# Kernel tuning notes

Measured on AMD Instinct MI355X. Metric: run time of the kernel, lower is better.

Reference implementation:

```python
import jax, jax.numpy as jnp
import numpy as np

N, C, T, V, S = 64, 64, 300, 25, 3
INTER = C // 4  # coff_embedding = 4
KER_T = 9      # temporal attention kernel
KER_V = V      # V=25 is odd -> spatial attention kernel = V, pad = (V-1)//2


def setup_inputs() -> dict:
    key = jax.random.key(0)
    ks = jax.random.split(key, 20)
    f = lambda k, s, scale=0.05: jax.random.normal(k, s, jnp.float32) * scale
    return {
        "x": jax.random.normal(ks[0], (N, C, T, V), jnp.float32),
        "A": f(ks[1], (S, V, V), 0.2),
        "alpha": jnp.array(0.1, jnp.float32),
        "Wa": f(ks[2], (S, INTER, C)), "ba": f(ks[3], (S, INTER)),
        "Wb": f(ks[4], (S, INTER, C)), "bb": f(ks[5], (S, INTER)),
        "Wd": f(ks[6], (S, C, C)),     "bd": f(ks[7], (S, C)),
        "bn_gamma": jnp.ones((C,), jnp.float32),
        "bn_beta": jnp.zeros((C,), jnp.float32),
        "bn_mean": f(ks[8], (C,)),
        "bn_var": jax.random.uniform(ks[9], (C,), jnp.float32) + 0.5,
        "Wsa": f(ks[10], (1, C, KER_V)), "bsa": f(ks[11], (1,)),
        "Wta": f(ks[12], (1, C, KER_T)), "bta": f(ks[13], (1,)),
        "Wfc1": f(ks[14], (C // 2, C)),  "bfc1": f(ks[15], (C // 2,)),
        "Wfc2": f(ks[16], (C, C // 2)),  "bfc2": f(ks[17], (C,)),
    }


def _conv1d(z, w, bias, pad):
    # z: [N, Cin, L], w: [Cout, Cin, K] -> [N, Cout, L]
    o = jax.lax.conv_general_dilated(z, w, (1,), [(pad, pad)],
                                     dimension_numbers=('NCH', 'OIH', 'NCH'))
    return o + bias[None, :, None]


def reference(x, A, alpha, Wa, ba, Wb, bb, Wd, bd,
              bn_gamma, bn_beta, bn_mean, bn_var,
              Wsa, bsa, Wta, bta, Wfc1, bfc1, Wfc2, bfc2):
    n, c, t, v = x.shape
    inter = Wa.shape[1]
    # adaptive adjacency per subset (1x1 convs = channel einsums)
    a = jnp.einsum('nctv,sic->nsitv', x, Wa) + ba[None, :, :, None, None]   # [N,S,inter,T,V]
    b = jnp.einsum('nctv,sic->nsitv', x, Wb) + bb[None, :, :, None, None]
    M = jnp.tanh(jnp.einsum('nsitv,nsitw->nsvw', a, b) / (inter * t))       # [N,S,V,V]
    G = A[None] + alpha * M
    # graph conv: x @ G per subset, then 1x1 conv_d, summed over subsets
    zp = jnp.einsum('nctv,nsvw->nsctw', x, G)                                # [N,S,C,T,V]
    y = jnp.einsum('nsctv,soc->notv', zp, Wd) + bd.sum(0)[None, :, None, None]
    # BN (eval) + residual (down = identity since in_c == out_c) + ReLU
    inv = bn_gamma / jnp.sqrt(bn_var + 1e-5)
    y = (y - bn_mean[None, :, None, None]) * inv[None, :, None, None] + bn_beta[None, :, None, None]
    y = jax.nn.relu(y + x)
    # spatial attention over joints
    se1 = jax.nn.sigmoid(_conv1d(y.mean(2), Wsa, bsa, (KER_V - 1) // 2))    # [N,1,V]
    y = y * se1[:, :, None, :] + y
    # temporal attention over frames
    se1 = jax.nn.sigmoid(_conv1d(y.mean(3), Wta, bta, (KER_T - 1) // 2))    # [N,1,T]
    y = y * se1[:, :, :, None] + y
    # channel attention (squeeze-excite)
    se = y.mean((2, 3))                                                      # [N,C]
    se2 = jax.nn.sigmoid(jax.nn.relu(se @ Wfc1.T + bfc1) @ Wfc2.T + bfc2)
    y = y * se2[:, :, None, None] + y
    return y
```

## Files before the change

### kernel.cpp

```cpp
#include <hip/hip_runtime.h>

typedef __bf16 bf16;
typedef bf16 bf16x8 __attribute__((ext_vector_type(8)));
typedef bf16 bf16x4 __attribute__((ext_vector_type(4)));
typedef float f32x4 __attribute__((ext_vector_type(4)));
typedef short s16x4 __attribute__((ext_vector_type(4)));

#define WS_XG    0u
#define WS_WAB   61505536u
#define WS_WD    61517824u
#define WS_COEFA 61542400u
#define WS_COEFB 61542656u
#define WS_GT    61542912u
#define WS_MPART 61936128u
#define WS_STP   61936128u
#define WS_SVP   68489728u
#define WS_SE1   74519040u
#define WS_SE2   74527232u
#define WS_SE3   74605056u

__device__ __forceinline__ f32x4 mfma16(bf16x8 a, bf16x8 b, f32x4 c) {
  return __builtin_amdgcn_mfma_f32_16x16x32_bf16(a, b, c, 0, 0, 0);
}

#if __has_builtin(__builtin_amdgcn_mfma_f32_16x16x16_bf16)
__device__ __forceinline__ f32x4 mfma16k(bf16x4 a, bf16x4 b, f32x4 c) {
  return __builtin_amdgcn_mfma_f32_16x16x16_bf16(a, b, c, 0, 0, 0);
}
#elif __has_builtin(__builtin_amdgcn_mfma_f32_16x16x16bf16_1k)
__device__ __forceinline__ f32x4 mfma16k(bf16x4 a, bf16x4 b, f32x4 c) {
  s16x4 ai = __builtin_bit_cast(s16x4, a);
  s16x4 bi = __builtin_bit_cast(s16x4, b);
  return __builtin_amdgcn_mfma_f32_16x16x16bf16_1k(ai, bi, c, 0, 0, 0);
}
#else
__device__ __forceinline__ f32x4 mfma16k(bf16x4 a, bf16x4 b, f32x4 c) {
  asm volatile("v_mfma_f32_16x16x16_bf16 %0, %1, %2, %0" : "+v"(c) : "v"(a), "v"(b));
  return c;
}
#endif

__global__ __launch_bounds__(256) void k_prep(
    const float* __restrict__ Wa, const float* __restrict__ Wb,
    const float* __restrict__ Wd, const float* __restrict__ bd,
    const float* __restrict__ gam, const float* __restrict__ bet,
    const float* __restrict__ mean, const float* __restrict__ var,
    char* __restrict__ ws) {
  bf16* wab = (bf16*)(ws + WS_WAB);
  bf16* wd  = (bf16*)(ws + WS_WD);
  float* cA = (float*)(ws + WS_COEFA);
  float* cB = (float*)(ws + WS_COEFB);
  int tid = threadIdx.x;
  for (int f = tid; f < 3*32*64; f += 256) {
    int s = f >> 11, r = (f >> 6) & 31, c = f & 63;
    float v = (r < 16) ? Wa[(s*16 + r)*64 + c] : Wb[(s*16 + (r-16))*64 + c];
    wab[f] = (bf16)v;
  }
  for (int f = tid; f < 3*64*64; f += 256) wd[f] = (bf16)Wd[f];
  if (tid < 64) {
    float bds = bd[tid] + bd[64+tid] + bd[128+tid];
    float iv = gam[tid] / sqrtf(var[tid] + 1e-5f);
    cA[tid] = iv;
    cB[tid] = (bds - mean[tid]) * iv + bet[tid];
  }
}

__global__ __launch_bounds__(256) void k_tr(
    const float* __restrict__ x, char* __restrict__ ws) {
  __shared__ __attribute__((aligned(16))) bf16 tile[64*204];
  const int tc = blockIdx.x, n = blockIdx.y, tid = threadIdx.x;
  const int t0 = tc*8;
  const int vmax = min(200, 7500 - t0*25);
  bf16* XG = (bf16*)(ws + WS_XG);
  #pragma unroll
  for (int it = 0; it < 13; ++it) {
    int u = it*256 + tid;
    if (u < 3200) {
      int c = u / 50, q = u % 50;
      int idx = 4*q;
      if (idx < vmax) {
        float4 val = *(const float4*)(x + (size_t)(n*64 + c)*7500 + t0*25 + idx);
        bf16x4 pk = {(bf16)val.x, (bf16)val.y, (bf16)val.z, (bf16)val.w};
        *(bf16x4*)&tile[c*204 + idx] = pk;
      }
    }
  }
  __syncthreads();
  #pragma unroll
  for (int it = 0; it < 7; ++it) {
    int u = it*256 + tid;
    if (u < 1600) {
      int c8 = u & 7, tv = u >> 3;
      int t = t0 + tv/25, v = tv % 25;
      if (t < 300) {
        bf16x8 pk;
        #pragma unroll
        for (int j = 0; j < 8; ++j) pk[j] = tile[(c8*8 + j)*204 + tv];
        *(bf16x8*)&XG[((size_t)(n*300 + t)*25 + v)*64 + c8*8] = pk;
      }
    }
  }
}

__global__ __launch_bounds__(256, 3) void k1_m(
    const float* __restrict__ ba_g, const float* __restrict__ bb_g,
    char* __restrict__ ws) {
  __shared__ float red[4][32][33];
  const int seg = blockIdx.x, n = blockIdx.y;
  const int tid = threadIdx.x;
  const int lane = tid & 63, wv = tid >> 6;
  const int l15 = lane & 15, l4 = lane >> 4;
  const int t0 = seg*19, tlen = min(19, 300 - t0);
  const bf16* XG  = (const bf16*)(ws + WS_XG);
  const bf16* wab = (const bf16*)(ws + WS_WAB);
  const f32x4 z4 = {0.f,0.f,0.f,0.f};

  bf16x8 Afr[6][2];
  float bias[6][4];
  #pragma unroll
  for (int rt = 0; rt < 6; ++rt) {
    const int s = rt >> 1, abk = rt & 1;
    #pragma unroll
    for (int kk = 0; kk < 2; ++kk)
      Afr[rt][kk] = *(const bf16x8*)&wab[(s*32 + abk*16 + l15)*64 + kk*32 + 8*l4];
    const float* bp = abk ? bb_g : ba_g;
    #pragma unroll
    for (int r = 0; r < 4; ++r) bias[rt][r] = bp[s*16 + 4*l4 + r];
  }
  f32x4 macc[3][2][2] = {};
  const int tb = (tlen*wv) >> 2, te = (tlen*(wv+1)) >> 2;

  for (int tl = tb; tl < te; ++tl) {
    const size_t rowb = (size_t)(n*300 + t0 + tl)*25;
    bf16x8 Bv[2][2];
    #pragma unroll
    for (int vt = 0; vt < 2; ++vt)
      #pragma unroll
      for (int kk = 0; kk < 2; ++kk)
        Bv[vt][kk] = *(const bf16x8*)&XG[(rowb + vt*16 + l15)*64 + kk*32 + 8*l4];
    #pragma unroll
    for (int s = 0; s < 3; ++s) {
      f32x4 acc[2][2];
      #pragma unroll
      for (int ab = 0; ab < 2; ++ab)
        #pragma unroll
        for (int vt = 0; vt < 2; ++vt) {
          f32x4 a = mfma16(Afr[2*s + ab][0], Bv[vt][0], z4);
          acc[ab][vt] = mfma16(Afr[2*s + ab][1], Bv[vt][1], a);
        }
      bf16x4 af[2], bf_[2];
      #pragma unroll
      for (int vt = 0; vt < 2; ++vt) {
        #pragma unroll
        for (int r = 0; r < 4; ++r) {
          af[vt][r]  = (bf16)(acc[0][vt][r] + bias[2*s][r]);
          bf_[vt][r] = (bf16)(acc[1][vt][r] + bias[2*s + 1][r]);
        }
      }
      #pragma unroll
      for (int vt = 0; vt < 2; ++vt)
        #pragma unroll
        for (int wt = 0; wt < 2; ++wt)
          macc[s][vt][wt] = mfma16k(af[vt], bf_[wt], macc[s][vt][wt]);
    }
  }
  float* mp = (float*)(ws + WS_MPART);
  #pragma unroll
  for (int s = 0; s < 3; ++s) {
    __syncthreads();
    #pragma unroll
    for (int vt = 0; vt < 2; ++vt)
      #pragma unroll
      for (int wt = 0; wt < 2; ++wt)
        #pragma unroll
        for (int r = 0; r < 4; ++r)
          red[wv][vt*16 + 4*l4 + r][wt*16 + l15] = macc[s][vt][wt][r];
    __syncthreads();
    for (int e = tid; e < 1024; e += 256) {
      int v = e >> 5, w = e & 31;
      float sum = red[0][v][w] + red[1][v][w] + red[2][v][w] + red[3][v][w];
      mp[(((n*16 + seg)*3 + s)*32 + v)*32 + w] = sum;
    }
  }
}

__global__ __launch_bounds__(256) void k1b_g(
    const float* __restrict__ A, const float* __restrict__ alp,
    char* __restrict__ ws) {
  int e = blockIdx.x*256 + threadIdx.x;
  int w = e & 31, v = (e >> 5) & 31;
  int s = (e >> 10) % 3, n = e / 3072;
  const float* mp = (const float*)(ws + WS_MPART);
  float m = 0.f;
  #pragma unroll
  for (int p = 0; p < 16; ++p)
    m += mp[(((n*16 + p)*3 + s)*32 + v)*32 + w];
  float g = 0.f;
  if (v < 25 && w < 25)
    g = A[(s*25 + v)*25 + w] + alp[0] * tanhf(m * (1.f/4800.f));
  bf16* gt = (bf16*)(ws + WS_GT);
  gt[((n*3 + s)*32 + w)*32 + v] = (bf16)g;
}

__global__ __launch_bounds__(256, 4) void k3_y(char* __restrict__ ws) {
  __shared__ __attribute__((aligned(16))) bf16 wdL[3*64*72];
  __shared__ __attribute__((aligned(16))) bf16 ULs[4*16*96];
  const int seg = blockIdx.x, n = blockIdx.y;
  const int tid = threadIdx.x, lane = tid & 63, wv = tid >> 6;
  const int l15 = lane & 15, l4 = lane >> 4;
  const int t0 = seg*19, tlen = min(19, 300 - t0);
  const bf16* XG = (const bf16*)(ws + WS_XG);
  bf16* YG = (bf16*)(ws + WS_XG);
  const bf16* wd = (const bf16*)(ws + WS_WD);
  const bf16* gt = (const bf16*)(ws + WS_GT);
  const float* cA = (const float*)(ws + WS_COEFA);
  const float* cB = (const float*)(ws + WS_COEFB);
  const f32x4 z4 = {0.f,0.f,0.f,0.f};
  bf16* UL = &ULs[wv*16*96];

  for (int f = tid; f < 1536; f += 256) {
    int row = f >> 3, c8 = f & 7;
    *(bf16x8*)&wdL[row*72 + c8*8] = *(const bf16x8*)&wd[row*64 + c8*8];
  }
  bf16x8 Gfr[2][3];
  #pragma unroll
  for (int wt = 0; wt < 2; ++wt)
    #pragma unroll
    for (int s = 0; s < 3; ++s)
      Gfr[wt][s] = *(const bf16x8*)&gt[((n*3 + s)*32 + wt*16 + l15)*32 + 8*l4];
  __syncthreads();

  const int tb = (tlen*wv) >> 2, te = (tlen*(wv+1)) >> 2;
  float st[4][2][4] = {};

  for (int tl = tb; tl < te; ++tl) {
    const size_t rowb = (size_t)(n*300 + t0 + tl)*25;
    bf16x8 Bv[2][2];
    #pragma unroll
    for (int vt = 0; vt < 2; ++vt)
      #pragma unroll
      for (int kk = 0; kk < 2; ++kk)
        Bv[vt][kk] = *(const bf16x8*)&XG[(rowb + vt*16 + l15)*64 + kk*32 + 8*l4];
    #pragma unroll
    for (int ot = 0; ot < 4; ++ot) {
      #pragma unroll
      for (int s = 0; s < 3; ++s) {
        bf16x8 W0 = *(const bf16x8*)&wdL[(s*64 + ot*16 + l15)*72 + 8*l4];
        bf16x8 W1 = *(const bf16x8*)&wdL[(s*64 + ot*16 + l15)*72 + 32 + 8*l4];
        #pragma unroll
        for (int vt = 0; vt < 2; ++vt) {
          f32x4 acc = mfma16(W0, Bv[vt][0], z4);
          acc = mfma16(W1, Bv[vt][1], acc);
          #pragma unroll
          for (int r = 0; r < 4; ++r)
            UL[(4*l4 + r)*96 + s*32 + vt*16 + l15] = (bf16)acc[r];
        }
      }
      f32x4 acc2[2] = {z4, z4};
      #pragma unroll
      for (int s = 0; s < 3; ++s) {
        bf16x8 Aa = *(const bf16x8*)&UL[l15*96 + s*32 + 8*l4];
        acc2[0] = mfma16(Aa, Gfr[0][s], acc2[0]);
        acc2[1] = mfma16(Aa, Gfr[1][s], acc2[1]);
      }
      const int o0 = ot*16 + 4*l4;
      const f32x4 cAr = *(const f32x4*)&cA[o0];
      const f32x4 cBr = *(const f32x4*)&cB[o0];
      #pragma unroll
      for (int wt = 0; wt < 2; ++wt) {
        const int w = wt*16 + l15;
        bf16x4 Rx = *(const bf16x4*)&XG[(rowb + w)*64 + o0];
        if (w < 25) {
          bf16x4 pk;
          #pragma unroll
          for (int r = 0; r < 4; ++r) {
            float val = fmaxf(acc2[wt][r]*cAr[r] + cBr[r] + (float)Rx[r], 0.f);
            pk[r] = (bf16)val;
            st[ot][wt][r] += val;
          }
          *(bf16x4*)&YG[(rowb + w)*64 + o0] = pk;
        }
      }
    }
  }
  float* LDSf = (float*)wdL;
  float* stp = (float*)(ws + WS_STP);
  #pragma unroll
  for (int half = 0; half < 2; ++half) {
    __syncthreads();
    #pragma unroll
    for (int ot2 = 0; ot2 < 2; ++ot2)
      #pragma unroll
      for (int wt = 0; wt < 2; ++wt)
        #pragma unroll
        for (int r = 0; r < 4; ++r)
          LDSf[wv*1056 + (ot2*16 + 4*l4 + r)*33 + wt*16 + l15] = st[half*2 + ot2][wt][r];
    __syncthreads();
    for (int e = tid; e < 800; e += 256) {
      int o = e / 25, w = e % 25;
      float sum = LDSf[o*33 + w] + LDSf[1056 + o*33 + w]
                + LDSf[2112 + o*33 + w] + LDSf[3168 + o*33 + w];
      stp[((n*16 + seg)*64 + half*32 + o)*25 + w] = sum;
    }
  }
}

__global__ __launch_bounds__(256) void k4_se1(
    const float* __restrict__ Wsa, const float* __restrict__ bsa,
    char* __restrict__ ws) {
  __shared__ float Sm[64][26];
  __shared__ float red[25][8];
  int n = blockIdx.x, tid = threadIdx.x;
  const float* stp = (const float*)(ws + WS_STP);
  for (int f = tid; f < 1600; f += 256) {
    int c = f / 25, v = f % 25;
    float s = 0.f;
    #pragma unroll
    for (int p = 0; p < 16; ++p) s += stp[((n*16 + p)*64 + c)*25 + v];
    Sm[c][v] = s * (1.f/300.f);
  }
  __syncthreads();
  float acc = 0.f;
  int v = tid >> 3, part = tid & 7;
  if (tid < 200) {
    for (int c = part; c < 64; c += 8) {
      #pragma unroll
      for (int k = 0; k < 25; ++k) {
        int vv = v + k - 12;
        if (vv >= 0 && vv < 25) acc += Wsa[c*25 + k] * Sm[c][vv];
      }
    }
    red[v][part] = acc;
  }
  __syncthreads();
  if (tid < 25) {
    float a = bsa[0];
    #pragma unroll
    for (int p = 0; p < 8; ++p) a += red[tid][p];
    ((float*)(ws + WS_SE1))[n*32 + tid] = 1.f + 1.f/(1.f + expf(-a));
  }
}

__global__ __launch_bounds__(256) void k5_sv(char* __restrict__ ws) {
  __shared__ float w1[25];
  const int tq = blockIdx.x, n = blockIdx.y;
  const int tid = threadIdx.x;
  const bf16* YG = (const bf16*)(ws + WS_XG);
  bf16* svp = (bf16*)(ws + WS_SVP);
  if (tid < 25) w1[tid] = ((const float*)(ws + WS_SE1))[n*32 + tid];
  __syncthreads();
  const int c8 = tid & 7, ts = tid >> 3;
  #pragma unroll
  for (int i = 0; i < 3; ++i) {
    int tl = i*32 + ts;
    if (tl < 75) {
      const int t = tq*75 + tl;
      float acc[8] = {};
      #pragma unroll
      for (int v = 0; v < 25; ++v) {
        bf16x8 yv = *(const bf16x8*)&YG[(((size_t)n*300 + t)*25 + v)*64 + c8*8];
        #pragma unroll
        for (int j = 0; j < 8; ++j) acc[j] += w1[v] * (float)yv[j];
      }
      bf16x8 pk;
      #pragma unroll
      for (int j = 0; j < 8; ++j) pk[j] = (bf16)acc[j];
      *(bf16x8*)&svp[((size_t)n*304 + t)*64 + c8*8] = pk;
    }
  }
}

__global__ __launch_bounds__(1024) void k_att2(
    const float* __restrict__ Wta, const float* __restrict__ bta,
    const float* __restrict__ Wfc1, const float* __restrict__ bfc1,
    const float* __restrict__ Wfc2, const float* __restrict__ bfc2,
    char* __restrict__ ws) {
  __shared__ bf16 Sv[64][304];
  __shared__ float WLa[576];
  __shared__ float redt[304][4];
  __shared__ float w2s[304];
  __shared__ float red2[64][16];
  __shared__ float mS[64];
  __shared__ float hS[32];
  const int n = blockIdx.x, tid = threadIdx.x;
  const bf16* svp = (const bf16*)(ws + WS_SVP);

  for (int u = tid; u < 300*64; u += 1024) {
    int t = u >> 6, c = u & 63;
    Sv[c][t] = svp[((size_t)n*304 + t)*64 + c];
  }
  for (int f = tid; f < 576; f += 1024) WLa[f] = Wta[f];
  __syncthreads();
  for (int u = tid; u < 1200; u += 1024) {
    int t = u >> 2, part = u & 3;
    float acc = 0.f;
    for (int c = part*16; c < part*16 + 16; ++c) {
      #pragma unroll
      for (int k = 0; k < 9; ++k) {
        int t2 = t + k - 4;
        if (t2 >= 0 && t2 < 300) acc += WLa[c*9 + k] * (float)Sv[c][t2];
      }
    }
    redt[t][part] = acc;
  }
  __syncthreads();
  if (tid < 300) {
    float a = (redt[tid][0] + redt[tid][1] + redt[tid][2] + redt[tid][3]) * (1.f/25.f) + bta[0];
    float f2 = 1.f + 1.f/(1.f + expf(-a));
    w2s[tid] = f2;
    ((float*)(ws + WS_SE2))[n*304 + tid] = f2;
  }
  __syncthreads();
  {
    int c = tid & 63, part = tid >> 6;
    int tb = part*19, te = min(tb + 19, 300);
    float acc = 0.f;
    for (int t = tb; t < te; ++t) acc += w2s[t] * (float)Sv[c][t];
    red2[c][part] = acc;
  }
  __syncthreads();
  if (tid < 64) {
    float mm = 0.f;
    #pragma unroll
    for (int p = 0; p < 16; ++p) mm += red2[tid][p];
    mS[tid] = mm * (1.f/7500.f);
  }
  __syncthreads();
  if (tid < 32) {
    float a = bfc1[tid];
    for (int c = 0; c < 64; ++c) a += Wfc1[tid*64 + c] * mS[c];
    hS[tid] = fmaxf(a, 0.f);
  }
  __syncthreads();
  if (tid < 64) {
    float a = bfc2[tid];
    #pragma unroll
    for (int j = 0; j < 32; ++j) a += Wfc2[tid*32 + j] * hS[j];
    ((float*)(ws + WS_SE3))[n*64 + tid] = 1.f + 1.f/(1.f + expf(-a));
  }
}

__global__ __launch_bounds__(256) void k7_scale(
    const char* __restrict__ ws, float* __restrict__ out) {
  __shared__ float tile[100*65];
  __shared__ float w3S[64];
  const int tc = blockIdx.x, n = blockIdx.y, tid = threadIdx.x;
  const bf16* YG = (const bf16*)(ws + WS_XG);
  const float* w1 = (const float*)(ws + WS_SE1) + n*32;
  const float* w2 = (const float*)(ws + WS_SE2) + n*304;
  if (tid < 64) w3S[tid] = ((const float*)(ws + WS_SE3))[n*64 + tid];
  const int tb = tc*4;
  __syncthreads();
  #pragma unroll
  for (int it = 0; it < 4; ++it) {
    int u = it*256 + tid;
    if (u < 800) {
      int c8 = u & 7, rest = u >> 3;
      int v = rest % 25, dt = rest / 25;
      int t = tb + dt;
      bf16x8 val = *(const bf16x8*)&YG[(((size_t)n*300 + t)*25 + v)*64 + c8*8];
      float sc = w1[v] * w2[t];
      #pragma unroll
      for (int j = 0; j < 8; ++j)
        tile[(dt*25 + v)*65 + c8*8 + j] = (float)val[j] * sc * w3S[c8*8 + j];
    }
  }
  __syncthreads();
  #pragma unroll
  for (int it = 0; it < 13; ++it) {
    int u = it*256 + tid;
    if (u < 3200) {
      int c = u / 50, q2 = u % 50;
      float2 o;
      o.x = tile[(2*q2)*65 + c];
      o.y = tile[(2*q2 + 1)*65 + c];
      *(float2*)&out[(size_t)(n*64 + c)*7500 + tb*25 + 2*q2] = o;
    }
  }
}

extern "C" void kernel_launch(void* const* d_in, const int* in_sizes, int n_in,
                              void* d_out, int out_size, void* d_ws, size_t ws_size,
                              hipStream_t stream) {
  const float* x    = (const float*)d_in[0];
  const float* A    = (const float*)d_in[1];
  const float* alp  = (const float*)d_in[2];
  const float* Wa   = (const float*)d_in[3];
  const float* ba   = (const float*)d_in[4];
  const float* Wb   = (const float*)d_in[5];
  const float* bb   = (const float*)d_in[6];
  const float* Wd   = (const float*)d_in[7];
  const float* bd   = (const float*)d_in[8];
  const float* gam  = (const float*)d_in[9];
  const float* bet  = (const float*)d_in[10];
  const float* mean = (const float*)d_in[11];
  const float* var  = (const float*)d_in[12];
  const float* Wsa  = (const float*)d_in[13];
  const float* bsa  = (const float*)d_in[14];
  const float* Wta  = (const float*)d_in[15];
  const float* bta  = (const float*)d_in[16];
  const float* Wfc1 = (const float*)d_in[17];
  const float* bfc1 = (const float*)d_in[18];
  const float* Wfc2 = (const float*)d_in[19];
  const float* bfc2 = (const float*)d_in[20];
  char* ws = (char*)d_ws;
  float* out = (float*)d_out;

  k_prep<<<dim3(1), dim3(256), 0, stream>>>(Wa, Wb, Wd, bd, gam, bet, mean, var, ws);
  k_tr<<<dim3(38, 64), dim3(256), 0, stream>>>(x, ws);
  k1_m<<<dim3(16, 64), dim3(256), 0, stream>>>(ba, bb, ws);
  k1b_g<<<dim3(768), dim3(256), 0, stream>>>(A, alp, ws);
  k3_y<<<dim3(16, 64), dim3(256), 0, stream>>>(ws);
  k4_se1<<<dim3(64), dim3(256), 0, stream>>>(Wsa, bsa, ws);
  k5_sv<<<dim3(4, 64), dim3(256), 0, stream>>>(ws);
  k_att2<<<dim3(64), dim3(1024), 0, stream>>>(Wta, bta, Wfc1, bfc1, Wfc2, bfc2, ws);
  k7_scale<<<dim3(75, 64), dim3(256), 0, stream>>>(ws, out);
}
```

Measured before the change: 236.6 us.

## Keep graph-conv intermediate in registers via transposed MFMA chaining; widen k5 grid

In k3_y the first MFMA now takes its operands in swapped order, so its output fragment can be fed straight into a 16x16x16 MFMA against the adjacency fragments. This removes the per-wave LDS staging buffer and its write/read round trip. The per-channel BN coefficients are hoisted into registers. The epilogue now does scalar bf16 residual loads and stores with a 64-element stride instead of 4-wide vector accesses, which risks poorer memory coalescing. Separately, k5_sv handles 30 frames per block over 10 blocks instead of 75 frames over 4 blocks, to raise parallelism.

```diff
diff --git a/kernel.cpp b/kernel.cpp
--- a/kernel.cpp
+++ b/kernel.cpp
@@ -204,7 +204,6 @@
 
 __global__ __launch_bounds__(256, 4) void k3_y(char* __restrict__ ws) {
   __shared__ __attribute__((aligned(16))) bf16 wdL[3*64*72];
-  __shared__ __attribute__((aligned(16))) bf16 ULs[4*16*96];
   const int seg = blockIdx.x, n = blockIdx.y;
   const int tid = threadIdx.x, lane = tid & 63, wv = tid >> 6;
   const int l15 = lane & 15, l4 = lane >> 4;
@@ -216,18 +215,22 @@
   const float* cA = (const float*)(ws + WS_COEFA);
   const float* cB = (const float*)(ws + WS_COEFB);
   const f32x4 z4 = {0.f,0.f,0.f,0.f};
-  bf16* UL = &ULs[wv*16*96];
 
   for (int f = tid; f < 1536; f += 256) {
     int row = f >> 3, c8 = f & 7;
     *(bf16x8*)&wdL[row*72 + c8*8] = *(const bf16x8*)&wd[row*64 + c8*8];
   }
-  bf16x8 Gfr[2][3];
-  #pragma unroll
-  for (int wt = 0; wt < 2; ++wt)
-    #pragma unroll
-    for (int s = 0; s < 3; ++s)
-      Gfr[wt][s] = *(const bf16x8*)&gt[((n*3 + s)*32 + wt*16 + l15)*32 + 8*l4];
+  bf16x4 GTk[3][2][2];
+  #pragma unroll
+  for (int s = 0; s < 3; ++s)
+    #pragma unroll
+    for (int vt = 0; vt < 2; ++vt)
+      #pragma unroll
+      for (int wt = 0; wt < 2; ++wt)
+        GTk[s][vt][wt] = *(const bf16x4*)&gt[((n*3 + s)*32 + wt*16 + l15)*32 + vt*16 + 4*l4];
+  float cAr[4], cBr[4];
+  #pragma unroll
+  for (int ot = 0; ot < 4; ++ot) { cAr[ot] = cA[ot*16 + l15]; cBr[ot] = cB[ot*16 + l15]; }
   __syncthreads();
 
   const int tb = (tlen*wv) >> 2, te = (tlen*(wv+1)) >> 2;
@@ -243,42 +246,37 @@
         Bv[vt][kk] = *(const bf16x8*)&XG[(rowb + vt*16 + l15)*64 + kk*32 + 8*l4];
     #pragma unroll
     for (int ot = 0; ot < 4; ++ot) {
+      bf16x4 uT[3][2];
       #pragma unroll
       for (int s = 0; s < 3; ++s) {
         bf16x8 W0 = *(const bf16x8*)&wdL[(s*64 + ot*16 + l15)*72 + 8*l4];
         bf16x8 W1 = *(const bf16x8*)&wdL[(s*64 + ot*16 + l15)*72 + 32 + 8*l4];
         #pragma unroll
         for (int vt = 0; vt < 2; ++vt) {
-          f32x4 acc = mfma16(W0, Bv[vt][0], z4);
-          acc = mfma16(W1, Bv[vt][1], acc);
+          f32x4 a = mfma16(Bv[vt][0], W0, z4);
+          a = mfma16(Bv[vt][1], W1, a);
           #pragma unroll
-          for (int r = 0; r < 4; ++r)
-            UL[(4*l4 + r)*96 + s*32 + vt*16 + l15] = (bf16)acc[r];
+          for (int r = 0; r < 4; ++r) uT[s][vt][r] = (bf16)a[r];
         }
       }
-      f32x4 acc2[2] = {z4, z4};
-      #pragma unroll
-      for (int s = 0; s < 3; ++s) {
-        bf16x8 Aa = *(const bf16x8*)&UL[l15*96 + s*32 + 8*l4];
-        acc2[0] = mfma16(Aa, Gfr[0][s], acc2[0]);
-        acc2[1] = mfma16(Aa, Gfr[1][s], acc2[1]);
-      }
-      const int o0 = ot*16 + 4*l4;
-      const f32x4 cAr = *(const f32x4*)&cA[o0];
-      const f32x4 cBr = *(const f32x4*)&cB[o0];
       #pragma unroll
       for (int wt = 0; wt < 2; ++wt) {
-        const int w = wt*16 + l15;
-        bf16x4 Rx = *(const bf16x4*)&XG[(rowb + w)*64 + o0];
-        if (w < 25) {
-          bf16x4 pk;
+        f32x4 acc = z4;
+        #pragma unroll
+        for (int s = 0; s < 3; ++s)
           #pragma unroll
-          for (int r = 0; r < 4; ++r) {
-            float val = fmaxf(acc2[wt][r]*cAr[r] + cBr[r] + (float)Rx[r], 0.f);
-            pk[r] = (bf16)val;
+          for (int vt = 0; vt < 2; ++vt)
+            acc = mfma16k(GTk[s][vt][wt], uT[s][vt], acc);
+        const int o = ot*16 + l15;
+        #pragma unroll
+        for (int r = 0; r < 4; ++r) {
+          const int w = wt*16 + 4*l4 + r;
+          if (w < 25) {
+            float rx = (float)XG[(rowb + w)*64 + o];
+            float val = fmaxf(acc[r]*cAr[ot] + cBr[ot] + rx, 0.f);
+            YG[(rowb + w)*64 + o] = (bf16)val;
             st[ot][wt][r] += val;
           }
-          *(bf16x4*)&YG[(rowb + w)*64 + o0] = pk;
         }
       }
     }
@@ -289,12 +287,14 @@
   for (int half = 0; half < 2; ++half) {
     __syncthreads();
     #pragma unroll
-    for (int ot2 = 0; ot2 < 2; ++ot2)
+    for (int otq = 0; otq < 2; ++otq) {
+      const int ot = half*2 + otq;
       #pragma unroll
       for (int wt = 0; wt < 2; ++wt)
         #pragma unroll
         for (int r = 0; r < 4; ++r)
-          LDSf[wv*1056 + (ot2*16 + 4*l4 + r)*33 + wt*16 + l15] = st[half*2 + ot2][wt][r];
+          LDSf[wv*1056 + (otq*16 + l15)*33 + wt*16 + 4*l4 + r] = st[ot][wt][r];
+    }
     __syncthreads();
     for (int e = tid; e < 800; e += 256) {
       int o = e / 25, w = e % 25;
@@ -350,23 +350,19 @@
   if (tid < 25) w1[tid] = ((const float*)(ws + WS_SE1))[n*32 + tid];
   __syncthreads();
   const int c8 = tid & 7, ts = tid >> 3;
-  #pragma unroll
-  for (int i = 0; i < 3; ++i) {
-    int tl = i*32 + ts;
-    if (tl < 75) {
-      const int t = tq*75 + tl;
-      float acc[8] = {};
-      #pragma unroll
-      for (int v = 0; v < 25; ++v) {
-        bf16x8 yv = *(const bf16x8*)&YG[(((size_t)n*300 + t)*25 + v)*64 + c8*8];
-        #pragma unroll
-        for (int j = 0; j < 8; ++j) acc[j] += w1[v] * (float)yv[j];
-      }
-      bf16x8 pk;
-      #pragma unroll
-      for (int j = 0; j < 8; ++j) pk[j] = (bf16)acc[j];
-      *(bf16x8*)&svp[((size_t)n*304 + t)*64 + c8*8] = pk;
-    }
+  if (ts < 30) {
+    const int t = tq*30 + ts;
+    float acc[8] = {};
+    #pragma unroll
+    for (int v = 0; v < 25; ++v) {
+      bf16x8 yv = *(const bf16x8*)&YG[(((size_t)n*300 + t)*25 + v)*64 + c8*8];
+      #pragma unroll
+      for (int j = 0; j < 8; ++j) acc[j] += w1[v] * (float)yv[j];
+    }
+    bf16x8 pk;
+    #pragma unroll
+    for (int j = 0; j < 8; ++j) pk[j] = (bf16)acc[j];
+    *(bf16x8*)&svp[((size_t)n*304 + t)*64 + c8*8] = pk;
   }
 }
 
@@ -512,7 +508,7 @@
   k1b_g<<<dim3(768), dim3(256), 0, stream>>>(A, alp, ws);
   k3_y<<<dim3(16, 64), dim3(256), 0, stream>>>(ws);
   k4_se1<<<dim3(64), dim3(256), 0, stream>>>(Wsa, bsa, ws);
-  k5_sv<<<dim3(4, 64), dim3(256), 0, stream>>>(ws);
+  k5_sv<<<dim3(10, 64), dim3(256), 0, stream>>>(ws);
   k_att2<<<dim3(64), dim3(1024), 0, stream>>>(Wta, bta, Wfc1, bfc1, Wfc2, bfc2, ws);
   k7_scale<<<dim3(75, 64), dim3(256), 0, stream>>>(ws, out);
 }
```

After: 415.7 us. 75.7% more time.
